# Optimization experiments

Measured on AMD Instinct MI355X. Metric: run time of the kernel, lower is better.

The kernel has to match this reference:

```python
import jax, jax.numpy as jnp
import numpy as np

N_NODES = 100000
N_EDGES = 1600000
IN_C, HID_C, OUT_C = 64, 64, 32


def gcn_conv(x, edge_index, W, b, n_nodes):
    """PyG GCNConv: add self-loops, symmetric norm, x @ W, scatter-add, + bias."""
    loop = jnp.arange(n_nodes, dtype=edge_index.dtype)
    src = jnp.concatenate([edge_index[0], loop])  # [E + N]
    dst = jnp.concatenate([edge_index[1], loop])
    # degree on destination (col) including self-loops -> deg >= 1
    deg = jax.ops.segment_sum(jnp.ones_like(dst, dtype=x.dtype), dst,
                              num_segments=n_nodes)
    dinv = jax.lax.rsqrt(deg)  # deg >= 1, no inf handling needed
    norm = dinv[src] * dinv[dst]  # [E + N]
    h = x @ W  # [N, C_out] -- transform first (small GEMM), then propagate
    msg = h[src] * norm[:, None]  # gather, memory-bound
    out = jax.ops.segment_sum(msg, dst, num_segments=n_nodes)  # scatter-add
    return out + b


def setup_inputs() -> dict:
    key = jax.random.key(0)
    k1, k2, k3, k4, k5 = jax.random.split(key, 5)
    x = jax.random.normal(k1, (N_NODES, IN_C), dtype=jnp.float32)
    edge_index = jax.random.randint(k2, (2, N_EDGES), 0, N_NODES, dtype=jnp.int64)
    s1 = 1.0 / np.sqrt(IN_C)
    s2 = 1.0 / np.sqrt(HID_C)
    W1 = jax.random.uniform(k3, (IN_C, HID_C), jnp.float32, -s1, s1)
    b1 = jnp.zeros((HID_C,), jnp.float32)
    W2 = jax.random.uniform(k4, (HID_C, OUT_C), jnp.float32, -s2, s2)
    b2 = jnp.zeros((OUT_C,), jnp.float32)
    return {"x": x, "edge_index": edge_index, "W1": W1, "b1": b1,
            "W2": W2, "b2": b2}


def reference(x, edge_index, W1, b1, W2, b2):
    n = x.shape[0]
    h = gcn_conv(x, edge_index, W1, b1, n)
    h = jax.nn.relu(h)
    out = gcn_conv(h, edge_index, W2, b2, n)
    return out
```

## Files before the change

kernel.cpp:

```cpp
#include <hip/hip_runtime.h>
#include <hip/hip_fp16.h>
#include <cstdint>
#include <cstddef>


#define CHUNK 4096
#define BKN 256
#define BKN_SHIFT 8
#define NCH_MAX 512
#define SCAP2 5120

__device__ __forceinline__ int load_edge(const int* e32, int idx, int is64) {
  if (is64) return (int)((const long long*)e32)[idx];
  return e32[idx];
}

__device__ __forceinline__ int detect_is64_block(const int* e32, int* s_tmp) {
  const int t = threadIdx.x;
  if (t < 64) {
    int v = e32[2 * t + 1];
    unsigned long long b = __ballot(v != 0);
    if (t == 0) *s_tmp = (b == 0ULL);
  }
  __syncthreads();
  return *s_tmp;
}

__global__ void k_histA(const int* __restrict__ e32, int E, int* __restrict__ histM,
                        int NBUCK) {
  __shared__ int lh[NCH_MAX];
  __shared__ int s_is64;
  const int c = blockIdx.x;
  const int t = threadIdx.x;
  const int is64 = detect_is64_block(e32, &s_is64);
  for (int i = t; i < NBUCK; i += 256) lh[i] = 0;
  __syncthreads();
  const int beg = c * CHUNK;
  const int n = min(CHUNK, E - beg);
  for (int i = t; i < n; i += 256) {
    int d = load_edge(e32, E + beg + i, is64);
    atomicAdd(&lh[d >> BKN_SHIFT], 1);
  }
  __syncthreads();
  for (int i = t; i < NBUCK; i += 256) histM[(size_t)c * NBUCK + i] = lh[i];
}

__device__ __forceinline__ void block_scan512(int* sh, int t) {
  for (int off = 1; off < 512; off <<= 1) {
    int i0 = t, i1 = t + 256;
    int v0 = sh[i0] + ((i0 >= off) ? sh[i0 - off] : 0);
    int v1 = sh[i1] + ((i1 >= off) ? sh[i1 - off] : 0);
    __syncthreads();
    sh[i0] = v0;
    sh[i1] = v1;
    __syncthreads();
  }
}

__global__ void k_colscanA(int* __restrict__ histM, int* __restrict__ btot,
                           int NCH, int NBUCK) {
  __shared__ int sh[NCH_MAX];
  const int b = blockIdx.x;
  const int t = threadIdx.x;
  for (int i = t; i < NCH_MAX; i += 256)
    sh[i] = (i < NCH) ? histM[(size_t)i * NBUCK + b] : 0;
  __syncthreads();
  block_scan512(sh, t);
  for (int i = t; i < NCH; i += 256)
    histM[(size_t)i * NBUCK + b] = (i == 0) ? 0 : sh[i - 1];
  if (t == 0) btot[b] = sh[NCH_MAX - 1];
}

__global__ void k_bscan(const int* __restrict__ btot, int* __restrict__ bbase,
                        int* __restrict__ rowptr, __half* __restrict__ h1,
                        __half* __restrict__ h2, int NBUCK, int N, int E) {
  __shared__ int sh[NCH_MAX];
  const int t = threadIdx.x;
  sh[t] = (t < NBUCK) ? btot[t] : 0;
  sh[t + 256] = (t + 256 < NBUCK) ? btot[t + 256] : 0;
  __syncthreads();
  block_scan512(sh, t);
  for (int i = t; i < NBUCK; i += 256) bbase[i] = (i == 0) ? 0 : sh[i - 1];
  if (t == 0) { bbase[NBUCK] = E; rowptr[N] = E; }
  if (t < 64) {
    h1[(size_t)N * 64 + t] = __float2half(0.f);
    if (t < 32) h2[(size_t)N * 32 + t] = __float2half(0.f);
  }
}

__global__ void k_scatter(const int* __restrict__ e32, int E, const int* __restrict__ histM,
                          const int* __restrict__ bbase, int NBUCK,
                          unsigned int* __restrict__ raw) {
  __shared__ int lcur[NCH_MAX];
  __shared__ int s_is64;
  const int c = blockIdx.x;
  const int t = threadIdx.x;
  const int is64 = detect_is64_block(e32, &s_is64);
  for (int i = t; i < NBUCK; i += 256)
    lcur[i] = histM[(size_t)c * NBUCK + i] + bbase[i];
  __syncthreads();
  const int beg = c * CHUNK;
  const int cnt = min(CHUNK, E - beg);
  for (int i = t; i < cnt; i += 256) {
    int s = load_edge(e32, beg + i, is64);
    int d = load_edge(e32, E + beg + i, is64);
    int pos = atomicAdd(&lcur[d >> BKN_SHIFT], 1);
    raw[pos] = ((unsigned int)(d & (BKN - 1)) << 23) | (unsigned int)s;
  }
}

__global__ void k_sort(const unsigned int* __restrict__ raw, const int* __restrict__ bbase,
                       int* __restrict__ rec, int* __restrict__ rowptr,
                       float* __restrict__ dinv, int N) {
  __shared__ int srec[SCAP2];
  __shared__ int sh[BKN];
  const int b = blockIdx.x;
  const int t = threadIdx.x;
  const int nodebase = b << BKN_SHIFT;
  const int base = bbase[b];
  const int end = bbase[b + 1];
  const int count = end - base;
  sh[t] = 0;
  __syncthreads();
  for (int i = t; i < count; i += 256) atomicAdd(&sh[raw[base + i] >> 23], 1);
  __syncthreads();
  const int deg = sh[t];
  for (int off = 1; off < 256; off <<= 1) {
    int add = (t >= off) ? sh[t - off] : 0;
    __syncthreads();
    sh[t] += add;
    __syncthreads();
  }
  const int excl = sh[t] - deg;
  const int n = nodebase + t;
  if (n < N) {
    rowptr[n] = base + excl;
    dinv[n] = rsqrtf((float)deg + 1.0f);
  }
  __syncthreads();
  sh[t] = excl;
  __syncthreads();
  if (count <= SCAP2) {
    for (int i = t; i < count; i += 256) {
      unsigned int r = raw[base + i];
      int pos = atomicAdd(&sh[r >> 23], 1);
      srec[pos] = (int)(r & 0x7FFFFFu);
    }
    __syncthreads();
    for (int i = t; i < count; i += 256) rec[base + i] = srec[i];
  } else {
    for (int i = t; i < count; i += 256) {
      unsigned int r = raw[base + i];
      int pos = atomicAdd(&sh[r >> 23], 1);
      rec[base + pos] = (int)(r & 0x7FFFFFu);
    }
  }
}

template <int CIN, int COUT>
__global__ void k_gemm(const float* __restrict__ Xv, const float* __restrict__ W,
                       const float* __restrict__ dinv, __half* __restrict__ H, int N) {
  constexpr int Q = COUT / 4;
  constexpr int NODES = 256 / Q;
  __shared__ float4 Ws[CIN * Q];
  __shared__ float Xs[NODES][CIN + 1];
  const int t = threadIdx.x;
  const int nodebase = blockIdx.x * NODES;

  const float4* W4 = (const float4*)W;
#pragma unroll
  for (int i = t; i < CIN * Q; i += 256) Ws[i] = W4[i];

  const float4* X4 = (const float4*)Xv;
#pragma unroll
  for (int i = t; i < NODES * (CIN / 4); i += 256) {
    int r = i / (CIN / 4);
    int k4 = i % (CIN / 4);
    int gr = nodebase + r;
    if (gr > N - 1) gr = N - 1;
    float4 v = X4[(size_t)gr * (CIN / 4) + k4];
    Xs[r][k4 * 4 + 0] = v.x;
    Xs[r][k4 * 4 + 1] = v.y;
    Xs[r][k4 * 4 + 2] = v.z;
    Xs[r][k4 * 4 + 3] = v.w;
  }
  __syncthreads();

  const int q = t % Q;
  const int nl = t / Q;
  const int n = nodebase + nl;
  float4 acc = make_float4(0.f, 0.f, 0.f, 0.f);
#pragma unroll 4
  for (int k = 0; k < CIN; ++k) {
    float xv = Xs[nl][k];
    float4 wv = Ws[k * Q + q];
    acc.x = fmaf(xv, wv.x, acc.x);
    acc.y = fmaf(xv, wv.y, acc.y);
    acc.z = fmaf(xv, wv.z, acc.z);
    acc.w = fmaf(xv, wv.w, acc.w);
  }
  if (n < N) {
    float dn = dinv[n];
    __half2* H2 = (__half2*)H;
    H2[(size_t)n * (COUT / 2) + 2 * q + 0] = __floats2half2_rn(acc.x * dn, acc.y * dn);
    H2[(size_t)n * (COUT / 2) + 2 * q + 1] = __floats2half2_rn(acc.z * dn, acc.w * dn);
  }
}

__device__ __forceinline__ void acc_row(float4 hv, float2& a0, float2& a1,
                                        float2& a2, float2& a3) {
  union { float f; __half2 h; } c0, c1, c2, c3;
  c0.f = hv.x; c1.f = hv.y; c2.f = hv.z; c3.f = hv.w;
  float2 f0 = __half22float2(c0.h), f1 = __half22float2(c1.h);
  float2 f2 = __half22float2(c2.h), f3 = __half22float2(c3.h);
  a0.x += f0.x; a0.y += f0.y;
  a1.x += f1.x; a1.y += f1.y;
  a2.x += f2.x; a2.y += f2.y;
  a3.x += f3.x; a3.y += f3.y;
}

#define RED2(v, m) { v.x += __shfl_xor(v.x, m); v.y += __shfl_xor(v.y, m); }

__global__ void k_prop64f(const __half2* __restrict__ H2, const int* __restrict__ rec,
                          const int* __restrict__ rowptr, const float* __restrict__ dinv,
                          const float* __restrict__ b1, const float* __restrict__ W2,
                          __half* __restrict__ h2, int N) {
  __shared__ float2 W2p[64 * 16];
  __shared__ float g1buf[4][4][68];
  const int t = threadIdx.x;
  const int lane = t & 63;
  const int wave = t >> 6;
  for (int i = t; i < 64 * 16; i += 256) {
    int c = i >> 4, k = i & 15;
    W2p[i] = make_float2(W2[c * 32 + k], W2[c * 32 + 16 + k]);
  }

  const int nl = lane >> 4;
  int n = blockIdx.x * 16 + wave * 4 + nl;
  if (n > N - 1) n = N - 1;
  const int g = (lane & 15) >> 3;
  const int l8 = lane & 7;
  const float di = dinv[n];
  const int beg = rowptr[n];
  const int end = rowptr[n + 1];
  const float4* H4 = (const float4*)H2;
  float2 a0 = {0.f, 0.f}, a1 = {0.f, 0.f}, a2 = {0.f, 0.f}, a3 = {0.f, 0.f};
  acc_row(H4[(size_t)(g == 0 ? n : N) * 8 + l8], a0, a1, a2, a3);
  for (int e = beg + g; e < end; e += 16) {
    int s0 = rec[e];
    int s1 = (e + 2  < end) ? rec[e + 2]  : N;
    int s2 = (e + 4  < end) ? rec[e + 4]  : N;
    int s3 = (e + 6  < end) ? rec[e + 6]  : N;
    int s4 = (e + 8  < end) ? rec[e + 8]  : N;
    int s5 = (e + 10 < end) ? rec[e + 10] : N;
    int s6 = (e + 12 < end) ? rec[e + 12] : N;
    int s7 = (e + 14 < end) ? rec[e + 14] : N;
    acc_row(H4[(size_t)s0 * 8 + l8], a0, a1, a2, a3);
    acc_row(H4[(size_t)s1 * 8 + l8], a0, a1, a2, a3);
    acc_row(H4[(size_t)s2 * 8 + l8], a0, a1, a2, a3);
    acc_row(H4[(size_t)s3 * 8 + l8], a0, a1, a2, a3);
    acc_row(H4[(size_t)s4 * 8 + l8], a0, a1, a2, a3);
    acc_row(H4[(size_t)s5 * 8 + l8], a0, a1, a2, a3);
    acc_row(H4[(size_t)s6 * 8 + l8], a0, a1, a2, a3);
    acc_row(H4[(size_t)s7 * 8 + l8], a0, a1, a2, a3);
  }
  RED2(a0, 8)  RED2(a1, 8)  RED2(a2, 8)  RED2(a3, 8)

  const float4* B4 = (const float4*)b1;
  float4 bb0 = B4[l8 * 2 + 0], bb1 = B4[l8 * 2 + 1];
  if (g == 0) {
    float4 r0 = make_float4(fmaxf(fmaf(a0.x, di, bb0.x), 0.f),
                            fmaxf(fmaf(a0.y, di, bb0.y), 0.f),
                            fmaxf(fmaf(a1.x, di, bb0.z), 0.f),
                            fmaxf(fmaf(a1.y, di, bb0.w), 0.f));
    float4 r1 = make_float4(fmaxf(fmaf(a2.x, di, bb1.x), 0.f),
                            fmaxf(fmaf(a2.y, di, bb1.y), 0.f),
                            fmaxf(fmaf(a3.x, di, bb1.z), 0.f),
                            fmaxf(fmaf(a3.y, di, bb1.w), 0.f));
    *(float4*)&g1buf[wave][nl][l8 * 8 + 0] = r0;
    *(float4*)&g1buf[wave][nl][l8 * 8 + 4] = r1;
  }
  __syncthreads();

  const int k = lane & 15;
  float o0 = 0.f, o1 = 0.f;
#pragma unroll
  for (int c4 = 0; c4 < 16; ++c4) {
    float4 r = *(const float4*)&g1buf[wave][nl][c4 * 4];
    float2 w0 = W2p[(c4 * 4 + 0) * 16 + k];
    float2 w1 = W2p[(c4 * 4 + 1) * 16 + k];
    float2 w2 = W2p[(c4 * 4 + 2) * 16 + k];
    float2 w3 = W2p[(c4 * 4 + 3) * 16 + k];
    o0 = fmaf(r.x, w0.x, o0); o1 = fmaf(r.x, w0.y, o1);
    o0 = fmaf(r.y, w1.x, o0); o1 = fmaf(r.y, w1.y, o1);
    o0 = fmaf(r.z, w2.x, o0); o1 = fmaf(r.z, w2.y, o1);
    o0 = fmaf(r.w, w3.x, o0); o1 = fmaf(r.w, w3.y, o1);
  }
  h2[(size_t)n * 32 + k]      = __float2half(o0 * di);
  h2[(size_t)n * 32 + k + 16] = __float2half(o1 * di);
}

__global__ void k_prop32(const __half2* __restrict__ H2, const int* __restrict__ rec,
                         const int* __restrict__ rowptr, const float* __restrict__ dinv,
                         const float* __restrict__ bias, float* __restrict__ out, int N) {
  const int lane = threadIdx.x & 63;
  const int wave = threadIdx.x >> 6;
  const int n = blockIdx.x * 32 + wave * 8 + (lane >> 3);
  if (n >= N) return;
  const int g = (lane & 7) >> 2;
  const int l4 = lane & 3;
  const float di = dinv[n];
  const int beg = rowptr[n];
  const int end = rowptr[n + 1];
  const float4* H4 = (const float4*)H2;
  float2 a0 = {0.f, 0.f}, a1 = {0.f, 0.f}, a2 = {0.f, 0.f}, a3 = {0.f, 0.f};
  acc_row(H4[(size_t)(g == 0 ? n : N) * 4 + l4], a0, a1, a2, a3);
  for (int e = beg + g; e < end; e += 16) {
    int s0 = rec[e];
    int s1 = (e + 2  < end) ? rec[e + 2]  : N;
    int s2 = (e + 4  < end) ? rec[e + 4]  : N;
    int s3 = (e + 6  < end) ? rec[e + 6]  : N;
    int s4 = (e + 8  < end) ? rec[e + 8]  : N;
    int s5 = (e + 10 < end) ? rec[e + 10] : N;
    int s6 = (e + 12 < end) ? rec[e + 12] : N;
    int s7 = (e + 14 < end) ? rec[e + 14] : N;
    acc_row(H4[(size_t)s0 * 4 + l4], a0, a1, a2, a3);
    acc_row(H4[(size_t)s1 * 4 + l4], a0, a1, a2, a3);
    acc_row(H4[(size_t)s2 * 4 + l4], a0, a1, a2, a3);
    acc_row(H4[(size_t)s3 * 4 + l4], a0, a1, a2, a3);
    acc_row(H4[(size_t)s4 * 4 + l4], a0, a1, a2, a3);
    acc_row(H4[(size_t)s5 * 4 + l4], a0, a1, a2, a3);
    acc_row(H4[(size_t)s6 * 4 + l4], a0, a1, a2, a3);
    acc_row(H4[(size_t)s7 * 4 + l4], a0, a1, a2, a3);
  }
  RED2(a0, 4)  RED2(a1, 4)  RED2(a2, 4)  RED2(a3, 4)
  if (g) return;
  const float4* B4 = (const float4*)bias;
  float4 b0 = B4[l4 * 2 + 0], b1 = B4[l4 * 2 + 1];
  ((float4*)out)[(size_t)n * 8 + l4 * 2 + 0] =
      make_float4(fmaf(a0.x, di, b0.x), fmaf(a0.y, di, b0.y),
                  fmaf(a1.x, di, b0.z), fmaf(a1.y, di, b0.w));
  ((float4*)out)[(size_t)n * 8 + l4 * 2 + 1] =
      make_float4(fmaf(a2.x, di, b1.x), fmaf(a2.y, di, b1.y),
                  fmaf(a3.x, di, b1.z), fmaf(a3.y, di, b1.w));
}

extern "C" void kernel_launch(void* const* d_in, const int* in_sizes, int n_in,
                              void* d_out, int out_size, void* d_ws, size_t ws_size,
                              hipStream_t stream) {
  (void)n_in; (void)out_size; (void)ws_size;
  const float* x = (const float*)d_in[0];
  const int* edges = (const int*)d_in[1];
  const float* W1 = (const float*)d_in[2];
  const float* b1 = (const float*)d_in[3];
  const float* W2 = (const float*)d_in[4];
  const float* b2 = (const float*)d_in[5];

  const int N = in_sizes[0] / 64;
  const int E = in_sizes[1] / 2;
  const int NCH = (E + CHUNK - 1) / CHUNK;
  const int NBUCK = (N + BKN - 1) / BKN;

  char* ws = (char*)d_ws;
  size_t off = 0;
  auto carve = [&](size_t bytes) -> void* {
    void* p = ws + off;
    off = (off + bytes + 255) & ~(size_t)255;
    return p;
  };
  int* rowptr        = (int*)carve((size_t)(N + 1) * 4);
  float* dinv        = (float*)carve((size_t)N * 4);
  int* btot          = (int*)carve((size_t)NBUCK * 4);
  int* bbase         = (int*)carve((size_t)(NBUCK + 1) * 4);
  int* histM         = (int*)carve((size_t)NCH * NBUCK * 4);
  unsigned int* raw  = (unsigned int*)carve((size_t)E * 4);
  int* rec           = (int*)carve(((size_t)E + 64) * 4);
  __half* h1         = (__half*)carve((size_t)(N + 1) * 64 * 2);
  __half* h2         = (__half*)carve((size_t)(N + 1) * 32 * 2);

  k_histA<<<NCH, 256, 0, stream>>>(edges, E, histM, NBUCK);
  k_colscanA<<<NBUCK, 256, 0, stream>>>(histM, btot, NCH, NBUCK);
  k_bscan<<<1, 256, 0, stream>>>(btot, bbase, rowptr, h1, h2, NBUCK, N, E);
  k_scatter<<<NCH, 256, 0, stream>>>(edges, E, histM, bbase, NBUCK, raw);
  k_sort<<<NBUCK, 256, 0, stream>>>(raw, bbase, rec, rowptr, dinv, N);

  k_gemm<64, 64><<<(N + 15) / 16, 256, 0, stream>>>(x, W1, dinv, h1, N);
  k_prop64f<<<(N + 15) / 16, 256, 0, stream>>>((const __half2*)h1, rec, rowptr,
                                               dinv, b1, W2, h2, N);
  k_prop32<<<(N + 31) / 32, 256, 0, stream>>>((const __half2*)h2, rec, rowptr, dinv,
                                              b2, (float*)d_out, N);
}
```

Before: 123.5 us.

## Merge CSR build kernels into one cooperative kernel with grid syncs

Replaces the five separate CSR-construction kernels (histogram, column scan, bucket scan, scatter, per-bucket sort) with a single cooperative kernel that separates phases with grid.sync(). Edge source/destination values are kept in shared memory between the histogram and scatter phases, so the edge list is read from global memory once instead of twice. This removes several launch gaps and the second edge read. In exchange it adds grid-wide barriers, uses more shared memory per block, and needs all NCH/NBUCK blocks (about 391) to be co-resident for the cooperative launch.

```diff
diff --git a/kernel.cpp b/kernel.cpp
--- a/kernel.cpp
+++ b/kernel.cpp
@@ -1,7 +1,10 @@
 #include <hip/hip_runtime.h>
 #include <hip/hip_fp16.h>
+#include <hip/hip_cooperative_groups.h>
 #include <cstdint>
 #include <cstddef>
+
+namespace cg = cooperative_groups;
 
 
 #define CHUNK 4096
@@ -15,36 +18,6 @@
   return e32[idx];
 }
 
-__device__ __forceinline__ int detect_is64_block(const int* e32, int* s_tmp) {
-  const int t = threadIdx.x;
-  if (t < 64) {
-    int v = e32[2 * t + 1];
-    unsigned long long b = __ballot(v != 0);
-    if (t == 0) *s_tmp = (b == 0ULL);
-  }
-  __syncthreads();
-  return *s_tmp;
-}
-
-__global__ void k_histA(const int* __restrict__ e32, int E, int* __restrict__ histM,
-                        int NBUCK) {
-  __shared__ int lh[NCH_MAX];
-  __shared__ int s_is64;
-  const int c = blockIdx.x;
-  const int t = threadIdx.x;
-  const int is64 = detect_is64_block(e32, &s_is64);
-  for (int i = t; i < NBUCK; i += 256) lh[i] = 0;
-  __syncthreads();
-  const int beg = c * CHUNK;
-  const int n = min(CHUNK, E - beg);
-  for (int i = t; i < n; i += 256) {
-    int d = load_edge(e32, E + beg + i, is64);
-    atomicAdd(&lh[d >> BKN_SHIFT], 1);
-  }
-  __syncthreads();
-  for (int i = t; i < NBUCK; i += 256) histM[(size_t)c * NBUCK + i] = lh[i];
-}
-
 __device__ __forceinline__ void block_scan512(int* sh, int t) {
   for (int off = 1; off < 512; off <<= 1) {
     int i0 = t, i1 = t + 256;
@@ -57,102 +30,128 @@
   }
 }
 
-__global__ void k_colscanA(int* __restrict__ histM, int* __restrict__ btot,
-                           int NCH, int NBUCK) {
-  __shared__ int sh[NCH_MAX];
+__global__ void k_build(const int* __restrict__ e32, int E, int* __restrict__ histM,
+                        int* __restrict__ btot, int* __restrict__ bbase,
+                        int* __restrict__ rowptr, float* __restrict__ dinv,
+                        unsigned int* __restrict__ raw, int* __restrict__ rec,
+                        __half* __restrict__ h1, __half* __restrict__ h2,
+                        int NCH, int NBUCK, int N) {
+  cg::grid_group grid = cg::this_grid();
+  __shared__ int s_flag;
+  __shared__ char smem[34816];
+  int* cacheD = (int*)smem;
+  int* cacheS = (int*)(smem + 16384);
+  int* aux    = (int*)(smem + 32768);
+  int* srec   = (int*)smem;
+  int* shE    = (int*)(smem + 20480);
+
+  const int t = threadIdx.x;
+  const int c = blockIdx.x;
   const int b = blockIdx.x;
-  const int t = threadIdx.x;
-  for (int i = t; i < NCH_MAX; i += 256)
-    sh[i] = (i < NCH) ? histM[(size_t)i * NBUCK + b] : 0;
+
+  if (t < 64) {
+    int v = e32[2 * t + 1];
+    unsigned long long bl = __ballot(v != 0);
+    if (t == 0) s_flag = (bl == 0ULL);
+  }
   __syncthreads();
-  block_scan512(sh, t);
-  for (int i = t; i < NCH; i += 256)
-    histM[(size_t)i * NBUCK + b] = (i == 0) ? 0 : sh[i - 1];
-  if (t == 0) btot[b] = sh[NCH_MAX - 1];
-}
-
-__global__ void k_bscan(const int* __restrict__ btot, int* __restrict__ bbase,
-                        int* __restrict__ rowptr, __half* __restrict__ h1,
-                        __half* __restrict__ h2, int NBUCK, int N, int E) {
-  __shared__ int sh[NCH_MAX];
-  const int t = threadIdx.x;
-  sh[t] = (t < NBUCK) ? btot[t] : 0;
-  sh[t + 256] = (t + 256 < NBUCK) ? btot[t + 256] : 0;
-  __syncthreads();
-  block_scan512(sh, t);
-  for (int i = t; i < NBUCK; i += 256) bbase[i] = (i == 0) ? 0 : sh[i - 1];
-  if (t == 0) { bbase[NBUCK] = E; rowptr[N] = E; }
-  if (t < 64) {
-    h1[(size_t)N * 64 + t] = __float2half(0.f);
-    if (t < 32) h2[(size_t)N * 32 + t] = __float2half(0.f);
-  }
-}
-
-__global__ void k_scatter(const int* __restrict__ e32, int E, const int* __restrict__ histM,
-                          const int* __restrict__ bbase, int NBUCK,
-                          unsigned int* __restrict__ raw) {
-  __shared__ int lcur[NCH_MAX];
-  __shared__ int s_is64;
-  const int c = blockIdx.x;
-  const int t = threadIdx.x;
-  const int is64 = detect_is64_block(e32, &s_is64);
-  for (int i = t; i < NBUCK; i += 256)
-    lcur[i] = histM[(size_t)c * NBUCK + i] + bbase[i];
-  __syncthreads();
+  const int is64 = s_flag;
+
   const int beg = c * CHUNK;
-  const int cnt = min(CHUNK, E - beg);
-  for (int i = t; i < cnt; i += 256) {
-    int s = load_edge(e32, beg + i, is64);
-    int d = load_edge(e32, E + beg + i, is64);
-    int pos = atomicAdd(&lcur[d >> BKN_SHIFT], 1);
-    raw[pos] = ((unsigned int)(d & (BKN - 1)) << 23) | (unsigned int)s;
-  }
-}
-
-__global__ void k_sort(const unsigned int* __restrict__ raw, const int* __restrict__ bbase,
-                       int* __restrict__ rec, int* __restrict__ rowptr,
-                       float* __restrict__ dinv, int N) {
-  __shared__ int srec[SCAP2];
-  __shared__ int sh[BKN];
-  const int b = blockIdx.x;
-  const int t = threadIdx.x;
-  const int nodebase = b << BKN_SHIFT;
-  const int base = bbase[b];
-  const int end = bbase[b + 1];
-  const int count = end - base;
-  sh[t] = 0;
-  __syncthreads();
-  for (int i = t; i < count; i += 256) atomicAdd(&sh[raw[base + i] >> 23], 1);
-  __syncthreads();
-  const int deg = sh[t];
-  for (int off = 1; off < 256; off <<= 1) {
-    int add = (t >= off) ? sh[t - off] : 0;
-    __syncthreads();
-    sh[t] += add;
-    __syncthreads();
-  }
-  const int excl = sh[t] - deg;
-  const int n = nodebase + t;
-  if (n < N) {
-    rowptr[n] = base + excl;
-    dinv[n] = rsqrtf((float)deg + 1.0f);
-  }
-  __syncthreads();
-  sh[t] = excl;
-  __syncthreads();
-  if (count <= SCAP2) {
-    for (int i = t; i < count; i += 256) {
-      unsigned int r = raw[base + i];
-      int pos = atomicAdd(&sh[r >> 23], 1);
-      srec[pos] = (int)(r & 0x7FFFFFu);
-    }
-    __syncthreads();
-    for (int i = t; i < count; i += 256) rec[base + i] = srec[i];
-  } else {
-    for (int i = t; i < count; i += 256) {
-      unsigned int r = raw[base + i];
-      int pos = atomicAdd(&sh[r >> 23], 1);
-      rec[base + pos] = (int)(r & 0x7FFFFFu);
+  const int cnt = (c < NCH) ? min(CHUNK, E - beg) : 0;
+
+  if (c < NCH) {
+    for (int i = t; i < NBUCK; i += 256) aux[i] = 0;
+    __syncthreads();
+    for (int i = t; i < cnt; i += 256) {
+      int s = load_edge(e32, beg + i, is64);
+      int d = load_edge(e32, E + beg + i, is64);
+      cacheS[i] = s;
+      cacheD[i] = d;
+      atomicAdd(&aux[d >> BKN_SHIFT], 1);
+    }
+    __syncthreads();
+    for (int i = t; i < NBUCK; i += 256) histM[(size_t)c * NBUCK + i] = aux[i];
+  }
+  grid.sync();
+
+  if (b < NBUCK) {
+    for (int i = t; i < NCH_MAX; i += 256)
+      aux[i] = (i < NCH) ? histM[(size_t)i * NBUCK + b] : 0;
+    __syncthreads();
+    block_scan512(aux, t);
+    for (int i = t; i < NCH; i += 256)
+      histM[(size_t)i * NBUCK + b] = (i == 0) ? 0 : aux[i - 1];
+    if (t == 0) btot[b] = aux[NCH_MAX - 1];
+  }
+  grid.sync();
+
+  if (blockIdx.x == 0) {
+    aux[t] = (t < NBUCK) ? btot[t] : 0;
+    aux[t + 256] = (t + 256 < NBUCK) ? btot[t + 256] : 0;
+    __syncthreads();
+    block_scan512(aux, t);
+    for (int i = t; i < NBUCK; i += 256) bbase[i] = (i == 0) ? 0 : aux[i - 1];
+    if (t == 0) { bbase[NBUCK] = E; rowptr[N] = E; }
+    if (t < 64) {
+      h1[(size_t)N * 64 + t] = __float2half(0.f);
+      if (t < 32) h2[(size_t)N * 32 + t] = __float2half(0.f);
+    }
+  }
+  grid.sync();
+
+  if (c < NCH) {
+    for (int i = t; i < NBUCK; i += 256)
+      aux[i] = histM[(size_t)c * NBUCK + i] + bbase[i];
+    __syncthreads();
+    for (int i = t; i < cnt; i += 256) {
+      int s = cacheS[i];
+      int d = cacheD[i];
+      int pos = atomicAdd(&aux[d >> BKN_SHIFT], 1);
+      raw[pos] = ((unsigned int)(d & (BKN - 1)) << 23) | (unsigned int)s;
+    }
+  }
+  grid.sync();
+
+  if (b < NBUCK) {
+    const int nodebase = b << BKN_SHIFT;
+    const int base = bbase[b];
+    const int end = bbase[b + 1];
+    const int count = end - base;
+    shE[t] = 0;
+    __syncthreads();
+    for (int i = t; i < count; i += 256) atomicAdd(&shE[raw[base + i] >> 23], 1);
+    __syncthreads();
+    const int deg = shE[t];
+    for (int off = 1; off < 256; off <<= 1) {
+      int add = (t >= off) ? shE[t - off] : 0;
+      __syncthreads();
+      shE[t] += add;
+      __syncthreads();
+    }
+    const int excl = shE[t] - deg;
+    const int n = nodebase + t;
+    if (n < N) {
+      rowptr[n] = base + excl;
+      dinv[n] = rsqrtf((float)deg + 1.0f);
+    }
+    __syncthreads();
+    shE[t] = excl;
+    __syncthreads();
+    if (count <= SCAP2) {
+      for (int i = t; i < count; i += 256) {
+        unsigned int r = raw[base + i];
+        int pos = atomicAdd(&shE[r >> 23], 1);
+        srec[pos] = (int)(r & 0x7FFFFFu);
+      }
+      __syncthreads();
+      for (int i = t; i < count; i += 256) rec[base + i] = srec[i];
+    } else {
+      for (int i = t; i < count; i += 256) {
+        unsigned int r = raw[base + i];
+        int pos = atomicAdd(&shE[r >> 23], 1);
+        rec[base + pos] = (int)(r & 0x7FFFFFu);
+      }
     }
   }
 }
@@ -360,6 +359,7 @@
   const int E = in_sizes[1] / 2;
   const int NCH = (E + CHUNK - 1) / CHUNK;
   const int NBUCK = (N + BKN - 1) / BKN;
+  const int GRID = (NCH > NBUCK) ? NCH : NBUCK;
 
   char* ws = (char*)d_ws;
   size_t off = 0;
@@ -378,11 +378,16 @@
   __half* h1         = (__half*)carve((size_t)(N + 1) * 64 * 2);
   __half* h2         = (__half*)carve((size_t)(N + 1) * 32 * 2);
 
-  k_histA<<<NCH, 256, 0, stream>>>(edges, E, histM, NBUCK);
-  k_colscanA<<<NBUCK, 256, 0, stream>>>(histM, btot, NCH, NBUCK);
-  k_bscan<<<1, 256, 0, stream>>>(btot, bbase, rowptr, h1, h2, NBUCK, N, E);
-  k_scatter<<<NCH, 256, 0, stream>>>(edges, E, histM, bbase, NBUCK, raw);
-  k_sort<<<NBUCK, 256, 0, stream>>>(raw, bbase, rec, rowptr, dinv, N);
+  {
+    int E_ = E, NCH_ = NCH, NBUCK_ = NBUCK, N_ = N;
+    const int* e_ = edges;
+    void* args[] = {(void*)&e_,     (void*)&E_,    (void*)&histM, (void*)&btot,
+                    (void*)&bbase,  (void*)&rowptr,(void*)&dinv,  (void*)&raw,
+                    (void*)&rec,    (void*)&h1,    (void*)&h2,    (void*)&NCH_,
+                    (void*)&NBUCK_, (void*)&N_};
+    hipLaunchCooperativeKernel((const void*)k_build, dim3(GRID), dim3(256),
+                               args, 0, stream);
+  }
 
   k_gemm<64, 64><<<(N + 15) / 16, 256, 0, stream>>>(x, W1, dinv, h1, N);
   k_prop64f<<<(N + 15) / 16, 256, 0, stream>>>((const __half2*)h1, rec, rowptr,
```

Result: slower. 327.6 us (+165.2%).
